# Performance work log

Measured on AMD Instinct MI355X. Metric: run time of the kernel, lower is better.

The kernel has to match this reference:

```python
import jax, jax.numpy as jnp
import numpy as np
import math

H = 65
W = 65
NH = 8
DIM_K = 512
DIM_Q = 512
DIM_HID = NH * DIM_K  # 4096; forced by V.view(bsz,-1,num_heads,dim_K)
RW = W // 2 + 1  # 33, rfft2 last-dim size


def _conv2d(x, w, pad):
    # x: NCHW, w: OIHW
    return jax.lax.conv_general_dilated(
        x, w, window_strides=(1, 1), padding=[(pad, pad), (pad, pad)],
        dimension_numbers=('NCHW', 'OIHW', 'NCHW'))


def _filter_branch(x, w1, w2, w3, Wd, bd):
    # x: (1, DIM_K, H, W)
    f = _conv2d(x, w1, 0)                                  # 1x1 conv
    f = _conv2d(jax.nn.relu(f), w2, 1) + f                 # 3x3 conv + residual
    f = jax.nn.relu(_conv2d(jax.nn.relu(f), w3, 0))        # 1x1 -> (1, NH, H, W)
    f = f.reshape(NH, H * W) @ Wd.T + bd                   # down-proj to (NH, 65*33)
    return f.reshape(NH, H, RW)


def setup_inputs() -> dict:
    key = jax.random.key(0)
    ks = jax.random.split(key, 20)
    s = 0.02
    f32 = jnp.float32
    inp = {
        'Q': jax.random.normal(ks[0], (1, 1, DIM_Q), f32),
        'K': jax.random.normal(ks[1], (1, DIM_K, H, W), f32),
        'Wq': jax.random.normal(ks[2], (DIM_HID, DIM_Q), f32) * s,
        'bq': jnp.zeros((DIM_HID,), f32),
        'Wk': jax.random.normal(ks[3], (DIM_HID, DIM_K), f32) * s,
        'bk': jnp.zeros((DIM_HID,), f32),
        'Wv': jax.random.normal(ks[4], (DIM_HID, DIM_K), f32) * s,
        'bv': jnp.zeros((DIM_HID,), f32),
        'Wo': jax.random.normal(ks[5], (DIM_K, DIM_HID), f32) * s,
        'bo': jnp.zeros((DIM_K,), f32),
        'amp1': jax.random.normal(ks[6], (DIM_K, DIM_K, 1, 1), f32) * 0.05,
        'amp2': jax.random.normal(ks[7], (DIM_K, DIM_K, 3, 3), f32) * 0.02,
        'amp3': jax.random.normal(ks[8], (NH, DIM_K, 1, 1), f32) * 0.05,
        'pha1': jax.random.normal(ks[9], (DIM_K, DIM_K, 1, 1), f32) * 0.05,
        'pha2': jax.random.normal(ks[10], (DIM_K, DIM_K, 3, 3), f32) * 0.02,
        'pha3': jax.random.normal(ks[11], (NH, DIM_K, 1, 1), f32) * 0.05,
        'Wd1': jax.random.normal(ks[12], (H * RW, H * W), f32) * s,
        'bd1': jnp.zeros((H * RW,), f32),
        'Wd2': jax.random.normal(ks[13], (H * RW, H * W), f32) * s,
        'bd2': jnp.zeros((H * RW,), f32),
    }
    return inp


def reference(Q, K, Wq, bq, Wk, bk, Wv, bv, Wo, bo,
              amp1, amp2, amp3, pha1, pha2, pha3, Wd1, bd1, Wd2, bd2):
    bsz, h, w = K.shape[0], K.shape[2], K.shape[3]
    dk = DIM_HID // NH
    qrt = K
    Kp = jnp.transpose(K, (0, 2, 3, 1))                      # (1, h, w, DIM_K)
    q = Q @ Wq.T + bq                                        # (1, 1, DIM_HID)
    k = Kp @ Wk.T + bk                                       # (1, h, w, DIM_HID)
    v = Kp @ Wv.T + bv
    q = q.reshape(bsz, -1, NH, dk).transpose(0, 2, 1, 3)     # (1, NH, 1, dk)
    k = k.reshape(bsz, -1, NH, dk).transpose(0, 2, 1, 3)     # (1, NH, h*w, dk)
    v = v.reshape(bsz, -1, NH, DIM_K).transpose(0, 2, 1, 3)  # (1, NH, h*w, DIM_K)
    A = jnp.einsum('bhqd,bhkd->bhqk', q, k) / math.sqrt(DIM_K)
    amp_F = _filter_branch(qrt, amp1, amp2, amp3, Wd1, bd1)  # (NH, h, w//2+1)
    pha_F = _filter_branch(qrt, pha1, pha2, pha3, Wd2, bd2)
    A = A.reshape(NH, h, w)
    Af = jnp.fft.rfft2(A, axes=(-2, -1))                     # backward norm (default)
    amp = amp_F * jnp.abs(Af)
    pha = pha_F * jnp.angle(Af)
    Af = jax.lax.complex(amp * jnp.cos(pha), amp * jnp.sin(pha))
    A = jnp.fft.irfft2(Af, s=(h, w), axes=(-2, -1))
    A = jax.nn.softmax(A.reshape(bsz, NH, 1, -1), axis=-1)   # (1, NH, 1, h*w)
    x = jnp.einsum('bhqk,bhkd->bhqd', A, v)                  # (1, NH, 1, DIM_K)
    x = x.reshape(1, NH * DIM_K)
    return x @ Wo.T + bo                                     # (1, DIM_K)
```

## Files before the change

kernel.cpp:

```cpp
#include <hip/hip_runtime.h>
#include <hip/hip_bf16.h>

#define NP 4225
#define PR 2145

typedef __attribute__((ext_vector_type(8))) short short8;
typedef __attribute__((ext_vector_type(4))) float f32x4;
typedef __attribute__((ext_vector_type(4))) unsigned int u32x4;

__device__ inline float bf2f(unsigned short u) {
    union { unsigned int i; float f; } x; x.i = ((unsigned int)u) << 16; return x.f;
}
__device__ inline unsigned short f2bf(float f) {
    union { float f; unsigned int i; } x; x.f = f;
    unsigned int r = x.i + 0x7fff + ((x.i >> 16) & 1);
    return (unsigned short)(r >> 16);
}
__device__ inline u32x4 relu8(u32x4 v) {
    #pragma unroll
    for (int i = 0; i < 4; i++) {
        unsigned int s = v[i] & 0x80008000u;
        v[i] &= ~((s >> 15) * 0xFFFFu);
    }
    return v;
}
__device__ inline void gl_lds16(const void* g, void* l) {
    __builtin_amdgcn_global_load_lds(
        (const __attribute__((address_space(1))) unsigned int*)g,
        (__attribute__((address_space(3))) unsigned int*)l,
        16, 0, 0);
}


__global__ __launch_bounds__(256) void k_qk4(const float* __restrict__ Q,
                                             const float* __restrict__ Wq,
                                             const float* __restrict__ bq,
                                             const float* __restrict__ Wk,
                                             float* __restrict__ qv,
                                             float* __restrict__ qkp,
                                             double* __restrict__ ctd, double* __restrict__ snd,
                                             float* __restrict__ ctf, float* __restrict__ stf)
{
    int bx = blockIdx.x, h = blockIdx.y, dz = blockIdx.z;
    int tid = threadIdx.x;
    if (bx == 1 && h == 0 && dz == 0 && tid < 65) {
        double ang = 6.283185307179586476925286766559 * (double)tid / 65.0;
        double cv = cos(ang), sv = sin(ang);
        ctd[tid] = cv; snd[tid] = sv;
        ctf[tid] = (float)cv; stf[tid] = (float)sv;
    }
    __shared__ float qs[32];
    int g = tid >> 3, l = tid & 7;
    int row = h * 512 + dz * 32 + g;
    float s = 0.f;
    for (int d = l; d < 512; d += 8) s += Q[d] * Wq[(size_t)row * 512 + d];
    s += __shfl_xor(s, 1);
    s += __shfl_xor(s, 2);
    s += __shfl_xor(s, 4);
    if (l == 0) qs[g] = s + bq[row];
    __syncthreads();
    if (bx == 0 && tid < 32) qv[h * 512 + dz * 32 + tid] = qs[tid];
    int c = bx * 256 + tid;
    float s2 = 0.f;
    #pragma unroll 8
    for (int d = 0; d < 32; d++)
        s2 += qs[d] * Wk[(size_t)(h * 512 + dz * 32 + d) * 512 + c];
    qkp[(dz * 8 + h) * 512 + c] = s2;
}

__global__ __launch_bounds__(256) void k_alogits3(const float* __restrict__ qkp,
                                                  const float* __restrict__ K,
                                                  float* __restrict__ Ap)
{
    __shared__ float sqk[8][16];
    int tid = threadIdx.x;
    int cz = blockIdx.y;
    if (tid < 128) {
        int hh = tid >> 4, cc = tid & 15;
        float s = 0.f;
        #pragma unroll
        for (int dz = 0; dz < 16; dz++) s += qkp[(dz * 8 + hh) * 512 + cz * 16 + cc];
        sqk[hh][cc] = s;
    }
    __syncthreads();
    int p = blockIdx.x * 256 + tid;
    bool ok = p < NP;
    float acc[8] = {};
    #pragma unroll
    for (int cc = 0; cc < 16; cc++) {
        float kv = ok ? K[(size_t)(cz * 16 + cc) * NP + p] : 0.f;
        #pragma unroll
        for (int h = 0; h < 8; h++) acc[h] += sqk[h][cc] * kv;
    }
    if (ok) {
        #pragma unroll
        for (int h = 0; h < 8; h++) Ap[(size_t)(cz * 8 + h) * NP + p] = acc[h];
    }
}

__global__ __launch_bounds__(128) void k_ared_fftA(const float* __restrict__ Ap,
                                                   const float* __restrict__ qv,
                                                   const float* __restrict__ bk,
                                                   const double* __restrict__ ctd,
                                                   const double* __restrict__ snd,
                                                   float* __restrict__ TrG, float* __restrict__ TiG)
{
    int y = blockIdx.x, h = blockIdx.y;
    int t = threadIdx.x;
    __shared__ float rowA[65];
    __shared__ double c65[65], s65[65];
    __shared__ float qbred[128];
    float qp = 0.f;
    for (int d = t; d < 512; d += 128) qp += qv[h * 512 + d] * bk[h * 512 + d];
    qbred[t] = qp;
    __syncthreads();
    for (int s = 64; s; s >>= 1) {
        if (t < s) qbred[t] += qbred[t + s];
        __syncthreads();
    }
    float qbh = qbred[0];
    if (t < 65) { c65[t] = ctd[t]; s65[t] = snd[t]; }
    const float sc = 0.04419417382415922f;
    if (t < 65) {
        int p = y * 65 + t;
        float s = 0.f;
        #pragma unroll 8
        for (int cz = 0; cz < 32; cz++) s += Ap[(size_t)(cz * 8 + h) * NP + p];
        rowA[t] = (s + qbh) * sc;
    }
    __syncthreads();
    int v = t;
    if (v < 33) {
        double sr = 0.0, si = 0.0;
        for (int x = 0; x < 65; x++) {
            int m = (v * x) % 65;
            double a = (double)rowA[x];
            sr += a * c65[m];
            si -= a * s65[m];
        }
        TrG[(h * 65 + y) * 33 + v] = (float)sr;
        TiG[(h * 65 + y) * 33 + v] = (float)si;
    }
}


__global__ __launch_bounds__(256) void k_cast2(const float* __restrict__ a,
                                               const float* __restrict__ b,
                                               unsigned short* __restrict__ o)
{
    int i = blockIdx.x * 256 + threadIdx.x;
    int br = blockIdx.y;
    const float* src = br ? b : a;
    int m = i >> 9, c = i & 511;
    int dst = (c & ~63) | ((c & 63) ^ ((m & 7) << 3));
    o[(size_t)br * 262144 + m * 512 + dst] = f2bf(src[i]);
}

__global__ __launch_bounds__(256) void k_packW2(const float* __restrict__ a,
                                                const float* __restrict__ b,
                                                unsigned short* __restrict__ o)
{
    int i = blockIdx.x * 256 + threadIdx.x;
    int br = blockIdx.y;
    int m = i >> 9, c = i & 511;
    const float* src = (br ? b : a) + (size_t)i * 9;
    unsigned short* dst = o + (size_t)br * 512 * 4608;
    int cs = (c & ~63) | ((c & 63) ^ ((m & 7) << 3));
    #pragma unroll
    for (int t = 0; t < 9; t++) dst[(size_t)m * 4608 + t * 512 + cs] = f2bf(src[t]);
}


__global__ __launch_bounds__(256) void k_conv1T(const float* __restrict__ K,
                                                const unsigned short* __restrict__ w1b2,
                                                unsigned short* __restrict__ f0b2)
{
    __shared__ unsigned short As[2][64 * 64];
    __shared__ unsigned short Bs[2][128 * 64];
    int tid = threadIdx.x;
    int bid = blockIdx.x;
    int u = bid & 7;
    int t = bid >> 3;
    int bmi = u * 9 + t % 9;
    if (bmi >= 67) return;
    int combo = t / 9;
    int bm = bmi * 64;
    int bn = (combo & 3) * 128;
    int br = combo >> 2;
    const unsigned short* w1 = w1b2 + (size_t)br * 262144;
    unsigned short* f0 = f0b2 + (size_t)br * NP * 512;
    int lane = tid & 63;
    int w = tid >> 6;
    int wp = (w >> 1) * 32, wm = (w & 1) * 64;
    int ct = tid >> 4, p4 = (tid & 15) * 4;

    bool okj[4];
    int colj[4];
    #pragma unroll
    for (int j = 0; j < 4; j++) {
        okj[j] = (bm + p4 + j) < NP;
        colj[j] = okj[j] ? (p4 + j) : (NP - 1 - bm);
    }

    f32x4 acc[2][4];
    #pragma unroll
    for (int i = 0; i < 2; i++)
        #pragma unroll
        for (int j = 0; j < 4; j++) acc[i][j] = (f32x4){0.f, 0.f, 0.f, 0.f};

    float aE[16], aO[16];

    auto loadA = [&](int kc, float (&ar)[16]) {
        int c0 = kc * 64;
        #pragma unroll
        for (int pass = 0; pass < 4; pass++) {
            int cl = pass * 16 + ct;
            const float* src = K + (size_t)(c0 + cl) * NP + bm;
            #pragma unroll
            for (int j = 0; j < 4; j++) ar[pass * 4 + j] = src[colj[j]];
        }
    };
    auto writeA = [&](int buf, float (&ar)[16]) {
        #pragma unroll
        for (int pass = 0; pass < 4; pass++) {
            int cl = pass * 16 + ct;
            #pragma unroll
            for (int j = 0; j < 4; j++) {
                int row = p4 + j;
                int byte = (row * 128 + cl * 2) ^ ((row & 7) << 4);
                float v = okj[j] ? ar[pass * 4 + j] : 0.f;
                *(unsigned short*)((char*)As[buf] + byte) = f2bf(v);
            }
        }
    };
    auto stageB = [&](int kc, int buf) {
        const unsigned short* gb = w1 + (size_t)kc * 64 + (lane & 7) * 8;
        #pragma unroll
        for (int j = 0; j < 4; j++) {
            int row = (w * 4 + j) * 8 + (lane >> 3);
            gl_lds16(gb + (size_t)(bn + row) * 512,
                     (char*)Bs[buf] + (w * 4 + j) * 1024);
        }
    };
    auto mfmaStep = [&](int buf) {
        __builtin_amdgcn_s_setprio(1);
        #pragma unroll
        for (int ks = 0; ks < 2; ks++) {
            short8 af[2], bfr[4];
            #pragma unroll
            for (int fi = 0; fi < 2; fi++) {
                int row = wp + fi * 16 + (lane & 15);
                int byte = row * 128 + ((ks * 64 + ((lane >> 4) * 16)) ^ ((row & 7) << 4));
                af[fi] = *(const short8*)((char*)As[buf] + byte);
            }
            #pragma unroll
            for (int fj = 0; fj < 4; fj++) {
                int n = wm + fj * 16 + (lane & 15);
                int byte = n * 128 + ((ks * 64 + ((lane >> 4) * 16)) ^ ((n & 7) << 4));
                bfr[fj] = *(const short8*)((char*)Bs[buf] + byte);
            }
            #pragma unroll
            for (int fi = 0; fi < 2; fi++)
                #pragma unroll
                for (int fj = 0; fj < 4; fj++)
                    acc[fi][fj] = __builtin_amdgcn_mfma_f32_16x16x32_bf16(af[fi], bfr[fj], acc[fi][fj], 0, 0, 0);
        }
        __builtin_amdgcn_s_setprio(0);
    };

    loadA(0, aE);
    loadA(1, aO);
    stageB(0, 0);
    writeA(0, aE);
    __syncthreads();
    #pragma unroll
    for (int ib = 0; ib < 4; ib++) {
        int s0 = 2 * ib;
        if (s0 + 1 < 8) stageB(s0 + 1, 1);
        if (s0 + 2 < 8) loadA(s0 + 2, aE);
        mfmaStep(0);
        if (s0 + 1 < 8) writeA(1, aO);
        __syncthreads();
        int s1 = s0 + 1;
        if (s1 + 1 < 8) stageB(s1 + 1, 0);
        if (s1 + 2 < 8) loadA(s1 + 2, aO);
        mfmaStep(1);
        if (s1 + 1 < 8) writeA(0, aE);
        __syncthreads();
    }
    #pragma unroll
    for (int fi = 0; fi < 2; fi++)
        #pragma unroll
        for (int r = 0; r < 4; r++) {
            int p = bm + wp + fi * 16 + (lane >> 4) * 4 + r;
            if (p >= NP) continue;
            #pragma unroll
            for (int fj = 0; fj < 4; fj++) {
                int m = bn + wm + fj * 16 + (lane & 15);
                f0[(size_t)p * 512 + m] = f2bf(acc[fi][fj][r]);
            }
        }
}

__global__ __launch_bounds__(256) void k_conv3T(const unsigned short* __restrict__ f0b2,
                                                const unsigned short* __restrict__ w2b2,
                                                const float* __restrict__ amp3,
                                                const float* __restrict__ pha3,
                                                float* __restrict__ F2)
{
    __shared__ unsigned short As[2][64 * 64];
    __shared__ unsigned short Bs[2][128 * 64];
    __shared__ float w3s[8 * 128];
    int tid = threadIdx.x;
    int bid = blockIdx.x;
    int u = bid & 7;
    int bmi = bid >> 3;
    if (bmi >= 67) return;
    int bm = bmi * 64;
    int bnq = u & 3;
    int bn = bnq * 128;
    int br = u >> 2;
    const unsigned short* f0 = f0b2 + (size_t)br * NP * 512;
    const unsigned short* w2 = w2b2 + (size_t)br * 512 * 4608;
    const float* w3 = br ? pha3 : amp3;
    for (int i = tid; i < 1024; i += 256) {
        int h = i >> 7, c = i & 127;
        w3s[i] = w3[h * 512 + bn + c];
    }
    int lane = tid & 63;
    int w = tid >> 6;
    int wp = (w >> 1) * 32, wm = (w & 1) * 64;
    int ra = tid >> 2, sa = tid & 3;
    int pA = bm + ra;
    int py = pA / 65, px = pA - py * 65;

    f32x4 acc[2][4];
    #pragma unroll
    for (int i = 0; i < 2; i++)
        #pragma unroll
        for (int j = 0; j < 4; j++) acc[i][j] = (f32x4){0.f, 0.f, 0.f, 0.f};

    u32x4 aE0, aE1, aO0, aO1;
    bool vE, vO;

    auto loadA = [&](int s, u32x4& a0, u32x4& a1, bool& vv) {
        int kc = s / 9, tap = s - kc * 9;
        int ky = tap / 3 - 1, kx = tap % 3 - 1;
        int sy = py + ky, sx = px + kx;
        bool valid = (pA < NP) && sy >= 0 && sy < 65 && sx >= 0 && sx < 65;
        int srow = valid ? (pA + ky * 65 + kx) : 0;
        const unsigned short* arow = f0 + (size_t)srow * 512 + kc * 64 + sa * 16;
        a0 = *(const u32x4*)arow;
        a1 = *(const u32x4*)(arow + 8);
        vv = valid;
    };
    auto writeA = [&](int buf, u32x4 a0, u32x4 a1, bool vv) {
        u32x4 z = {0, 0, 0, 0};
        u32x4 w0 = vv ? relu8(a0) : z;
        u32x4 w1 = vv ? relu8(a1) : z;
        int ab = ra * 128 + sa * 32;
        int swz = (ra & 7) << 4;
        *(u32x4*)((char*)As[buf] + (ab ^ swz)) = w0;
        *(u32x4*)((char*)As[buf] + ((ab + 16) ^ swz)) = w1;
    };
    auto stageB = [&](int s, int buf) {
        int kc = s / 9, tap = s - kc * 9;
        const unsigned short* gb = w2 + (size_t)tap * 512 + kc * 64 + (lane & 7) * 8;
        #pragma unroll
        for (int j = 0; j < 4; j++) {
            int row = (w * 4 + j) * 8 + (lane >> 3);
            gl_lds16(gb + (size_t)(bn + row) * 4608,
                     (char*)Bs[buf] + (w * 4 + j) * 1024);
        }
    };
    auto mfmaStep = [&](int buf) {
        __builtin_amdgcn_s_setprio(1);
        #pragma unroll
        for (int ks = 0; ks < 2; ks++) {
            short8 af[2], bfr[4];
            #pragma unroll
            for (int fi = 0; fi < 2; fi++) {
                int row = wp + fi * 16 + (lane & 15);
                int byte = row * 128 + ((ks * 64 + ((lane >> 4) * 16)) ^ ((row & 7) << 4));
                af[fi] = *(const short8*)((char*)As[buf] + byte);
            }
            #pragma unroll
            for (int fj = 0; fj < 4; fj++) {
                int n = wm + fj * 16 + (lane & 15);
                int byte = n * 128 + ((ks * 64 + ((lane >> 4) * 16)) ^ ((n & 7) << 4));
                bfr[fj] = *(const short8*)((char*)Bs[buf] + byte);
            }
            #pragma unroll
            for (int fi = 0; fi < 2; fi++)
                #pragma unroll
                for (int fj = 0; fj < 4; fj++)
                    acc[fi][fj] = __builtin_amdgcn_mfma_f32_16x16x32_bf16(af[fi], bfr[fj], acc[fi][fj], 0, 0, 0);
        }
        __builtin_amdgcn_s_setprio(0);
    };

    loadA(0, aE0, aE1, vE);
    loadA(1, aO0, aO1, vO);
    stageB(0, 0);
    writeA(0, aE0, aE1, vE);
    __syncthreads();
    for (int ib = 0; ib < 36; ib++) {
        int s0 = 2 * ib;
        if (s0 + 1 < 72) stageB(s0 + 1, 1);
        if (s0 + 2 < 72) loadA(s0 + 2, aE0, aE1, vE);
        mfmaStep(0);
        if (s0 + 1 < 72) writeA(1, aO0, aO1, vO);
        __syncthreads();
        int s1 = s0 + 1;
        if (s1 + 1 < 72) stageB(s1 + 1, 0);
        if (s1 + 2 < 72) loadA(s1 + 2, aO0, aO1, vO);
        mfmaStep(1);
        if (s1 + 1 < 72) writeA(0, aE0, aE1, vE);
        __syncthreads();
    }
    #pragma unroll
    for (int fi = 0; fi < 2; fi++)
        #pragma unroll
        for (int r = 0; r < 4; r++) {
            int row = wp + fi * 16 + (lane >> 4) * 4 + r;
            int p = bm + row;
            #pragma unroll
            for (int fj = 0; fj < 4; fj++) {
                int mcol = wm + fj * 16 + (lane & 15);
                float v = 0.f;
                if (p < NP)
                    v = fmaxf(acc[fi][fj][r] + bf2f(f0[(size_t)p * 512 + bn + mcol]), 0.f);
                int byte = (row * 256 + mcol * 2) ^ ((row & 7) << 4);
                *(unsigned short*)((char*)Bs[0] + byte) = f2bf(v);
            }
        }
    __syncthreads();
    int pl = tid >> 2, qc = tid & 3;
    float a8[8] = {};
    #pragma unroll 4
    for (int jj = 0; jj < 16; jj++) {
        int c = qc * 32 + jj * 2;
        int byte = (pl * 256 + c * 2) ^ ((pl & 7) << 4);
        unsigned int uu = *(const unsigned int*)((char*)Bs[0] + byte);
        float v0 = bf2f((unsigned short)(uu & 0xFFFF));
        float v1 = bf2f((unsigned short)(uu >> 16));
        #pragma unroll
        for (int h = 0; h < 8; h++)
            a8[h] += w3s[h * 128 + c] * v0 + w3s[h * 128 + c + 1] * v1;
    }
    #pragma unroll
    for (int h = 0; h < 8; h++) {
        a8[h] += __shfl_xor(a8[h], 1);
        a8[h] += __shfl_xor(a8[h], 2);
    }
    int p = bm + pl;
    if (qc == 0 && p < NP) {
        #pragma unroll
        for (int h = 0; h < 8; h++)
            atomicAdd(&F2[(size_t)(br * 8 + h) * NP + p], a8[h]);
    }
}

__global__ __launch_bounds__(256) void k_down(const float* __restrict__ F2,
                                              const float* __restrict__ Wd1,
                                              const float* __restrict__ bd1,
                                              const float* __restrict__ Wd2,
                                              const float* __restrict__ bd2,
                                              float* __restrict__ Fa,
                                              float* __restrict__ Fp)
{
    int wid = threadIdx.x >> 6, lane = threadIdx.x & 63;
    int j = blockIdx.x * 4 + wid;
    if (j >= PR) return;
    int br = blockIdx.y;
    const float* Wd = br ? Wd2 : Wd1;
    const float* bd = br ? bd2 : bd1;
    const float* F2b = F2 + (size_t)br * 8 * NP;
    float* Fo = br ? Fp : Fa;
    const float* wr = Wd + (size_t)j * NP;
    float acc[8] = {};
    for (int p = lane; p < NP; p += 64) {
        float wv = wr[p];
        #pragma unroll
        for (int h = 0; h < 8; h++) acc[h] += wv * fmaxf(F2b[h * NP + p], 0.f);
    }
    #pragma unroll
    for (int h = 0; h < 8; h++) {
        #pragma unroll
        for (int off = 32; off; off >>= 1) acc[h] += __shfl_down(acc[h], off);
    }
    if (lane == 0) {
        float b = bd[j];
        #pragma unroll
        for (int h = 0; h < 8; h++) Fo[h * PR + j] = acc[h] + b;
    }
}


__global__ __launch_bounds__(128) void k_fftBC(const float* __restrict__ TrG,
                                               const float* __restrict__ TiG,
                                               const float* __restrict__ Fa,
                                               const float* __restrict__ Fp,
                                               const double* __restrict__ ctd,
                                               const double* __restrict__ snd,
                                               const float* __restrict__ ctf,
                                               const float* __restrict__ stf,
                                               float* __restrict__ CrG, float* __restrict__ CiG)
{
    int v = blockIdx.x, h = blockIdx.y;
    int t = threadIdx.x;
    __shared__ float TrS[65], TiS[65];
    __shared__ float BrS[65], BiS[65];
    __shared__ double c65[65], s65[65];
    __shared__ float cf[65], sf[65];
    if (t < 65) {
        TrS[t] = TrG[(h * 65 + t) * 33 + v];
        TiS[t] = TiG[(h * 65 + t) * 33 + v];
        c65[t] = ctd[t]; s65[t] = snd[t];
        cf[t] = ctf[t]; sf[t] = stf[t];
    }
    __syncthreads();
    int uu = t;
    if (uu < 65) {
        double sr = 0.0, si = 0.0;
        for (int y = 0; y < 65; y++) {
            int m = (uu * y) % 65;
            double c = c65[m], s = s65[m];
            double tr = (double)TrS[y], ti = (double)TiS[y];
            sr += tr * c + ti * s;
            si += ti * c - tr * s;
        }
        float re = (float)sr, im = (float)si;
        float mag = sqrtf(re * re + im * im);
        float ang = atan2f(im, re);
        int o = uu * 33 + v;
        float amp = Fa[h * PR + o] * mag;
        float ph  = Fp[h * PR + o] * ang;
        float sn, cn;
        sincosf(ph, &sn, &cn);
        BrS[uu] = amp * cn;
        BiS[uu] = amp * sn;
    }
    __syncthreads();
    int y = t;
    if (y < 65) {
        float sr = 0.f, si = 0.f;
        for (int u2 = 0; u2 < 65; u2++) {
            int m = (u2 * y) % 65;
            float c = cf[m], s = sf[m];
            float ar = BrS[u2], ai = BiS[u2];
            sr += ar * c - ai * s;
            si += ai * c + ar * s;
        }
        CrG[(h * 65 + y) * 33 + v] = sr;
        CiG[(h * 65 + y) * 33 + v] = si;
    }
}

__global__ __launch_bounds__(128) void k_fftD(const float* __restrict__ CrG,
                                              const float* __restrict__ CiG,
                                              const float* __restrict__ ctf,
                                              const float* __restrict__ stf,
                                              float* __restrict__ A2)
{
    int y = blockIdx.x, h = blockIdx.y;
    int t = threadIdx.x;
    __shared__ float CrS[33], CiS[33];
    __shared__ float c65[65], s65[65];
    if (t < 33) {
        CrS[t] = CrG[(h * 65 + y) * 33 + t];
        CiS[t] = CiG[(h * 65 + y) * 33 + t];
    }
    if (t < 65) { c65[t] = ctf[t]; s65[t] = stf[t]; }
    __syncthreads();
    int x = t;
    if (x < 65) {
        float s = CrS[0];
        for (int v = 1; v < 33; v++) {
            int m = (v * x) % 65;
            s += 2.f * (CrS[v] * c65[m] - CiS[v] * s65[m]);
        }
        A2[h * NP + y * 65 + x] = s * (1.f / 4225.f);
    }
}

__global__ __launch_bounds__(1024) void k_softmax(const float* __restrict__ A2,
                                                  float* __restrict__ Wsm)
{
    int h = blockIdx.x, tid = threadIdx.x;
    __shared__ float red[1024];
    float mx = -3.0e38f;
    for (int i = tid; i < NP; i += 1024) mx = fmaxf(mx, A2[h * NP + i]);
    red[tid] = mx; __syncthreads();
    for (int s = 512; s; s >>= 1) {
        if (tid < s) red[tid] = fmaxf(red[tid], red[tid + s]);
        __syncthreads();
    }
    mx = red[0]; __syncthreads();
    float sum = 0.f;
    for (int i = tid; i < NP; i += 1024) sum += expf(A2[h * NP + i] - mx);
    red[tid] = sum; __syncthreads();
    for (int s = 512; s; s >>= 1) {
        if (tid < s) red[tid] += red[tid + s];
        __syncthreads();
    }
    float inv = 1.f / red[0];
    for (int i = tid; i < NP; i += 1024) Wsm[h * NP + i] = expf(A2[h * NP + i] - mx) * inv;
}

__global__ __launch_bounds__(256) void k_t(const float* __restrict__ K,
                                           const float* __restrict__ Wsm,
                                           float* __restrict__ t)
{
    int wid = threadIdx.x >> 6, lane = threadIdx.x & 63;
    int c = blockIdx.x * 4 + wid;
    float acc[8] = {};
    for (int p = lane; p < NP; p += 64) {
        float kv = K[(size_t)c * NP + p];
        #pragma unroll
        for (int h = 0; h < 8; h++) acc[h] += kv * Wsm[h * NP + p];
    }
    #pragma unroll
    for (int h = 0; h < 8; h++) {
        #pragma unroll
        for (int off = 32; off; off >>= 1) acc[h] += __shfl_down(acc[h], off);
    }
    if (lane == 0) {
        #pragma unroll
        for (int h = 0; h < 8; h++) t[h * 512 + c] = acc[h];
    }
}

__global__ __launch_bounds__(256) void k_x(const float* __restrict__ t,
                                           const float* __restrict__ Wv,
                                           const float* __restrict__ bv,
                                           float* __restrict__ x)
{
    int wid = threadIdx.x >> 6, lane = threadIdx.x & 63;
    int hd = blockIdx.x * 4 + wid;
    int h = hd >> 9;
    float s = 0.f;
    for (int c = lane; c < 512; c += 64) s += t[h * 512 + c] * Wv[(size_t)hd * 512 + c];
    #pragma unroll
    for (int off = 32; off; off >>= 1) s += __shfl_down(s, off);
    if (lane == 0) x[hd] = s + bv[hd];
}

__global__ __launch_bounds__(256) void k_out(const float* __restrict__ x,
                                             const float* __restrict__ Wo,
                                             const float* __restrict__ bo,
                                             float* __restrict__ out)
{
    int wid = threadIdx.x >> 6, lane = threadIdx.x & 63;
    int j = blockIdx.x * 4 + wid;
    float s = 0.f;
    for (int i = lane; i < 4096; i += 64) s += x[i] * Wo[(size_t)j * 4096 + i];
    #pragma unroll
    for (int off = 32; off; off >>= 1) s += __shfl_down(s, off);
    if (lane == 0) out[j] = s + bo[j];
}

extern "C" void kernel_launch(void* const* d_in, const int* in_sizes, int n_in,
                              void* d_out, int out_size, void* d_ws, size_t ws_size,
                              hipStream_t stream)
{
    (void)in_sizes; (void)n_in; (void)out_size; (void)ws_size;
    const float* Q    = (const float*)d_in[0];
    const float* K    = (const float*)d_in[1];
    const float* Wq   = (const float*)d_in[2];
    const float* bq   = (const float*)d_in[3];
    const float* Wk   = (const float*)d_in[4];
    const float* bk   = (const float*)d_in[5];
    const float* Wv   = (const float*)d_in[6];
    const float* bv   = (const float*)d_in[7];
    const float* Wo   = (const float*)d_in[8];
    const float* bo   = (const float*)d_in[9];
    const float* amp1 = (const float*)d_in[10];
    const float* amp2 = (const float*)d_in[11];
    const float* amp3 = (const float*)d_in[12];
    const float* pha1 = (const float*)d_in[13];
    const float* pha2 = (const float*)d_in[14];
    const float* pha3 = (const float*)d_in[15];
    const float* Wd1  = (const float*)d_in[16];
    const float* bd1  = (const float*)d_in[17];
    const float* Wd2  = (const float*)d_in[18];
    const float* bd2  = (const float*)d_in[19];
    float* out = (float*)d_out;

    char* w = (char*)d_ws;
    auto alloc = [&](size_t bytes) { char* p = w; w += (bytes + 255) & ~(size_t)255; return p; };
    float* qv   = (float*)alloc(4096 * 4);
    float* qkp  = (float*)alloc(16 * 8 * 512 * 4);
    unsigned short* w1b2 = (unsigned short*)alloc((size_t)2 * 512 * 512 * 2);
    unsigned short* w2b2 = (unsigned short*)alloc((size_t)2 * 512 * 4608 * 2);
    unsigned short* f0b2 = (unsigned short*)alloc((size_t)2 * NP * 512 * 2);
    float* F2   = (float*)alloc((size_t)2 * 8 * NP * 4);
    float* Fa   = (float*)alloc(8 * PR * 4);
    float* Fp   = (float*)alloc(8 * PR * 4);
    double* ctd = (double*)alloc(65 * 8);
    double* snd = (double*)alloc(65 * 8);
    float* ctf  = (float*)alloc(65 * 4);
    float* stf  = (float*)alloc(65 * 4);
    float* TrG  = (float*)alloc(8 * PR * 4);
    float* TiG  = (float*)alloc(8 * PR * 4);
    float* CrG  = (float*)alloc(8 * PR * 4);
    float* CiG  = (float*)alloc(8 * PR * 4);
    float* Ap   = (float*)w2b2;
    {
        char* s2 = (char*)f0b2;
        auto alias = [&](size_t bytes) { char* p = s2; s2 += (bytes + 255) & ~(size_t)255; return p; };
        float* A2  = (float*)alias(8 * NP * 4);
        float* wsm = (float*)alias(8 * NP * 4);
        float* tt  = (float*)alias(4096 * 4);
        float* xx  = (float*)alias(4096 * 4);

        hipMemsetAsync(F2, 0, (size_t)2 * 8 * NP * 4, stream);

        k_qk4<<<dim3(2, 8, 16), 256, 0, stream>>>(Q, Wq, bq, Wk, qv, qkp, ctd, snd, ctf, stf);
        k_alogits3<<<dim3(17, 32), 256, 0, stream>>>(qkp, K, Ap);
        k_ared_fftA<<<dim3(65, 8), 128, 0, stream>>>(Ap, qv, bk, ctd, snd, TrG, TiG);

        k_cast2<<<dim3(1024, 2), 256, 0, stream>>>(amp1, pha1, w1b2);
        k_packW2<<<dim3(1024, 2), 256, 0, stream>>>(amp2, pha2, w2b2);

        k_conv1T<<<576, 256, 0, stream>>>(K, w1b2, f0b2);
        k_conv3T<<<536, 256, 0, stream>>>(f0b2, w2b2, amp3, pha3, F2);
        k_down<<<dim3(537, 2), 256, 0, stream>>>(F2, Wd1, bd1, Wd2, bd2, Fa, Fp);

        k_fftBC<<<dim3(33, 8), 128, 0, stream>>>(TrG, TiG, Fa, Fp, ctd, snd, ctf, stf, CrG, CiG);
        k_fftD<<<dim3(65, 8), 128, 0, stream>>>(CrG, CiG, ctf, stf, A2);
        k_softmax<<<8, 1024, 0, stream>>>(A2, wsm);
        k_t<<<128, 256, 0, stream>>>(K, wsm, tt);
        k_x<<<1024, 256, 0, stream>>>(tt, Wv, bv, xx);
        k_out<<<128, 256, 0, stream>>>(xx, Wo, bo, out);
    }
}
```

Baseline: 257.3 us.

## Split softmax across blocks with atomics and defer normalization; merge weight-prep kernels

The single-block-per-head softmax is replaced. k_fftD now computes a per-head max through an order-preserving atomicMax, and a new k_sm2 spreads exponentiation and sum reduction across many blocks with atomicAdd. Division by the sum is deferred into k_x. k_t is split over 4 pixel chunks with atomic accumulation to raise parallelism, and the two weight cast kernels are merged into one launch. This removes a low-occupancy serial kernel and some launch overhead, but adds atomics, a non-deterministic summation order, and a larger memset.

```diff
diff --git a/kernel.cpp b/kernel.cpp
--- a/kernel.cpp
+++ b/kernel.cpp
@@ -29,6 +29,13 @@
         (const __attribute__((address_space(1))) unsigned int*)g,
         (__attribute__((address_space(3))) unsigned int*)l,
         16, 0, 0);
+}
+__device__ inline unsigned int fenc(float x) {
+    unsigned int u = __float_as_uint(x);
+    return (u & 0x80000000u) ? ~u : (u | 0x80000000u);
+}
+__device__ inline float fdec(unsigned int e) {
+    return (e & 0x80000000u) ? __uint_as_float(e & 0x7FFFFFFFu) : __uint_as_float(~e);
 }
 
 
@@ -144,30 +151,26 @@
 }
 
 
-__global__ __launch_bounds__(256) void k_cast2(const float* __restrict__ a,
-                                               const float* __restrict__ b,
-                                               unsigned short* __restrict__ o)
-{
-    int i = blockIdx.x * 256 + threadIdx.x;
-    int br = blockIdx.y;
-    const float* src = br ? b : a;
-    int m = i >> 9, c = i & 511;
-    int dst = (c & ~63) | ((c & 63) ^ ((m & 7) << 3));
-    o[(size_t)br * 262144 + m * 512 + dst] = f2bf(src[i]);
-}
-
-__global__ __launch_bounds__(256) void k_packW2(const float* __restrict__ a,
-                                                const float* __restrict__ b,
-                                                unsigned short* __restrict__ o)
+__global__ __launch_bounds__(256) void k_wprep(const float* __restrict__ a1,
+                                               const float* __restrict__ p1,
+                                               const float* __restrict__ a2,
+                                               const float* __restrict__ p2,
+                                               unsigned short* __restrict__ w1b2,
+                                               unsigned short* __restrict__ w2b2)
 {
     int i = blockIdx.x * 256 + threadIdx.x;
     int br = blockIdx.y;
     int m = i >> 9, c = i & 511;
-    const float* src = (br ? b : a) + (size_t)i * 9;
-    unsigned short* dst = o + (size_t)br * 512 * 4608;
     int cs = (c & ~63) | ((c & 63) ^ ((m & 7) << 3));
-    #pragma unroll
-    for (int t = 0; t < 9; t++) dst[(size_t)m * 4608 + t * 512 + cs] = f2bf(src[t]);
+    if (blockIdx.z == 0) {
+        const float* src = br ? p1 : a1;
+        w1b2[(size_t)br * 262144 + m * 512 + cs] = f2bf(src[i]);
+    } else {
+        const float* src = (br ? p2 : a2) + (size_t)i * 9;
+        unsigned short* dst = w2b2 + (size_t)br * 512 * 4608;
+        #pragma unroll
+        for (int t = 0; t < 9; t++) dst[(size_t)m * 4608 + t * 512 + cs] = f2bf(src[t]);
+    }
 }
 
 
@@ -561,12 +564,14 @@
                                               const float* __restrict__ CiG,
                                               const float* __restrict__ ctf,
                                               const float* __restrict__ stf,
-                                              float* __restrict__ A2)
+                                              float* __restrict__ A2,
+                                              unsigned int* __restrict__ mxb)
 {
     int y = blockIdx.x, h = blockIdx.y;
     int t = threadIdx.x;
     __shared__ float CrS[33], CiS[33];
     __shared__ float c65[65], s65[65];
+    __shared__ float red[128];
     if (t < 33) {
         CrS[t] = CrG[(h * 65 + y) * 33 + t];
         CiS[t] = CiG[(h * 65 + y) * 33 + t];
@@ -574,38 +579,46 @@
     if (t < 65) { c65[t] = ctf[t]; s65[t] = stf[t]; }
     __syncthreads();
     int x = t;
+    float s = -3.0e38f;
     if (x < 65) {
-        float s = CrS[0];
+        s = CrS[0];
         for (int v = 1; v < 33; v++) {
             int m = (v * x) % 65;
             s += 2.f * (CrS[v] * c65[m] - CiS[v] * s65[m]);
         }
-        A2[h * NP + y * 65 + x] = s * (1.f / 4225.f);
-    }
-}
-
-__global__ __launch_bounds__(1024) void k_softmax(const float* __restrict__ A2,
-                                                  float* __restrict__ Wsm)
-{
-    int h = blockIdx.x, tid = threadIdx.x;
-    __shared__ float red[1024];
-    float mx = -3.0e38f;
-    for (int i = tid; i < NP; i += 1024) mx = fmaxf(mx, A2[h * NP + i]);
-    red[tid] = mx; __syncthreads();
-    for (int s = 512; s; s >>= 1) {
-        if (tid < s) red[tid] = fmaxf(red[tid], red[tid + s]);
+        s *= (1.f / 4225.f);
+        A2[h * NP + y * 65 + x] = s;
+    }
+    red[t] = s;
+    __syncthreads();
+    for (int st = 64; st; st >>= 1) {
+        if (t < st) red[t] = fmaxf(red[t], red[t + st]);
         __syncthreads();
     }
-    mx = red[0]; __syncthreads();
-    float sum = 0.f;
-    for (int i = tid; i < NP; i += 1024) sum += expf(A2[h * NP + i] - mx);
-    red[tid] = sum; __syncthreads();
-    for (int s = 512; s; s >>= 1) {
-        if (tid < s) red[tid] += red[tid + s];
+    if (t == 0) atomicMax(&mxb[h], fenc(red[0]));
+}
+
+__global__ __launch_bounds__(256) void k_sm2(const float* __restrict__ A2,
+                                             const unsigned int* __restrict__ mxb,
+                                             float* __restrict__ Wsm,
+                                             float* __restrict__ sumb)
+{
+    int h = blockIdx.y, t = threadIdx.x;
+    int p = blockIdx.x * 256 + t;
+    float mx = fdec(mxb[h]);
+    float w = 0.f;
+    if (p < NP) {
+        w = expf(A2[h * NP + p] - mx);
+        Wsm[h * NP + p] = w;
+    }
+    __shared__ float red[256];
+    red[t] = w;
+    __syncthreads();
+    for (int st = 128; st; st >>= 1) {
+        if (t < st) red[t] += red[t + st];
         __syncthreads();
     }
-    float inv = 1.f / red[0];
-    for (int i = tid; i < NP; i += 1024) Wsm[h * NP + i] = expf(A2[h * NP + i] - mx) * inv;
+    if (t == 0) atomicAdd(&sumb[h], red[0]);
 }
 
 __global__ __launch_bounds__(256) void k_t(const float* __restrict__ K,
@@ -614,8 +627,11 @@
 {
     int wid = threadIdx.x >> 6, lane = threadIdx.x & 63;
     int c = blockIdx.x * 4 + wid;
+    int yq = blockIdx.y;
+    int p0 = yq * 1057;
+    int p1 = p0 + 1057; if (p1 > NP) p1 = NP;
     float acc[8] = {};
-    for (int p = lane; p < NP; p += 64) {
+    for (int p = p0 + lane; p < p1; p += 64) {
         float kv = K[(size_t)c * NP + p];
         #pragma unroll
         for (int h = 0; h < 8; h++) acc[h] += kv * Wsm[h * NP + p];
@@ -627,11 +643,12 @@
     }
     if (lane == 0) {
         #pragma unroll
-        for (int h = 0; h < 8; h++) t[h * 512 + c] = acc[h];
+        for (int h = 0; h < 8; h++) atomicAdd(&t[h * 512 + c], acc[h]);
     }
 }
 
 __global__ __launch_bounds__(256) void k_x(const float* __restrict__ t,
+                                           const float* __restrict__ sumb,
                                            const float* __restrict__ Wv,
                                            const float* __restrict__ bv,
                                            float* __restrict__ x)
@@ -643,7 +660,7 @@
     for (int c = lane; c < 512; c += 64) s += t[h * 512 + c] * Wv[(size_t)hd * 512 + c];
     #pragma unroll
     for (int off = 32; off; off >>= 1) s += __shfl_down(s, off);
-    if (lane == 0) x[hd] = s + bv[hd];
+    if (lane == 0) x[hd] = s / sumb[h] + bv[hd];
 }
 
 __global__ __launch_bounds__(256) void k_out(const float* __restrict__ x,
@@ -695,6 +712,10 @@
     unsigned short* w2b2 = (unsigned short*)alloc((size_t)2 * 512 * 4608 * 2);
     unsigned short* f0b2 = (unsigned short*)alloc((size_t)2 * NP * 512 * 2);
     float* F2   = (float*)alloc((size_t)2 * 8 * NP * 4);
+    unsigned int* mxb = (unsigned int*)alloc(8 * 4);
+    float* sumb = (float*)alloc(8 * 4);
+    float* tt   = (float*)alloc(4096 * 4);
+    char* zend  = w;
     float* Fa   = (float*)alloc(8 * PR * 4);
     float* Fp   = (float*)alloc(8 * PR * 4);
     double* ctd = (double*)alloc(65 * 8);
@@ -711,27 +732,25 @@
         auto alias = [&](size_t bytes) { char* p = s2; s2 += (bytes + 255) & ~(size_t)255; return p; };
         float* A2  = (float*)alias(8 * NP * 4);
         float* wsm = (float*)alias(8 * NP * 4);
-        float* tt  = (float*)alias(4096 * 4);
         float* xx  = (float*)alias(4096 * 4);
 
-        hipMemsetAsync(F2, 0, (size_t)2 * 8 * NP * 4, stream);
+        hipMemsetAsync(F2, 0, (size_t)(zend - (char*)F2), stream);
 
         k_qk4<<<dim3(2, 8, 16), 256, 0, stream>>>(Q, Wq, bq, Wk, qv, qkp, ctd, snd, ctf, stf);
         k_alogits3<<<dim3(17, 32), 256, 0, stream>>>(qkp, K, Ap);
         k_ared_fftA<<<dim3(65, 8), 128, 0, stream>>>(Ap, qv, bk, ctd, snd, TrG, TiG);
 
-        k_cast2<<<dim3(1024, 2), 256, 0, stream>>>(amp1, pha1, w1b2);
-        k_packW2<<<dim3(1024, 2), 256, 0, stream>>>(amp2, pha2, w2b2);
+        k_wprep<<<dim3(1024, 2, 2), 256, 0, stream>>>(amp1, pha1, amp2, pha2, w1b2, w2b2);
 
         k_conv1T<<<576, 256, 0, stream>>>(K, w1b2, f0b2);
         k_conv3T<<<536, 256, 0, stream>>>(f0b2, w2b2, amp3, pha3, F2);
         k_down<<<dim3(537, 2), 256, 0, stream>>>(F2, Wd1, bd1, Wd2, bd2, Fa, Fp);
 
         k_fftBC<<<dim3(33, 8), 128, 0, stream>>>(TrG, TiG, Fa, Fp, ctd, snd, ctf, stf, CrG, CiG);
-        k_fftD<<<dim3(65, 8), 128, 0, stream>>>(CrG, CiG, ctf, stf, A2);
-        k_softmax<<<8, 1024, 0, stream>>>(A2, wsm);
-        k_t<<<128, 256, 0, stream>>>(K, wsm, tt);
-        k_x<<<1024, 256, 0, stream>>>(tt, Wv, bv, xx);
+        k_fftD<<<dim3(65, 8), 128, 0, stream>>>(CrG, CiG, ctf, stf, A2, mxb);
+        k_sm2<<<dim3(17, 8), 256, 0, stream>>>(A2, mxb, wsm, sumb);
+        k_t<<<dim3(128, 4), 256, 0, stream>>>(K, wsm, tt);
+        k_x<<<1024, 256, 0, stream>>>(tt, sumb, Wv, bv, xx);
         k_out<<<128, 256, 0, stream>>>(xx, Wo, bo, out);
     }
 }
```

Result: faster. 243.2 us (median of 2 runs) (-5.5%).
